# Kernel optimization log

Measured on AMD Instinct MI355X. Metric: run time of the kernel, lower is better.

Reference implementation:

```python
import jax, jax.numpy as jnp
import numpy as np

N_NODES = 50000
N_EDGES = 800000
D_IN = 128
D_HID = 200
D_OUT = 64
EPS = 0.0  # initial_eps, train_eps=False


def setup_inputs() -> dict:
    key = jax.random.key(0)
    ks = jax.random.split(key, 8)
    x = jax.random.normal(ks[0], (N_NODES, D_IN), dtype=jnp.float32)
    edge_row = jax.random.randint(ks[1], (N_EDGES,), 0, N_NODES)
    edge_col = jax.random.randint(ks[2], (N_EDGES,), 0, N_NODES)
    edge_val = jax.random.uniform(ks[3], (N_EDGES,), dtype=jnp.float32)
    W1 = jax.random.normal(ks[4], (D_IN, D_HID), dtype=jnp.float32) * 0.05
    b1 = jnp.zeros((D_HID,), dtype=jnp.float32)
    W2 = jax.random.normal(ks[5], (D_HID, D_OUT), dtype=jnp.float32) * 0.05
    b2 = jnp.zeros((D_OUT,), dtype=jnp.float32)
    return {"x": x, "edge_row": edge_row, "edge_col": edge_col,
            "edge_val": edge_val, "W1": W1, "b1": b1, "W2": W2, "b2": b2}


def reference(x, edge_row, edge_col, edge_val, W1, b1, W2, b2):
    # SpMM: agg[i] = sum_e val[e] * x[col[e]] for edges with row[e] == i
    msgs = edge_val[:, None] * x[edge_col]            # [E, D_IN] gather
    agg = jax.ops.segment_sum(msgs, edge_row, num_segments=N_NODES)  # [N, D_IN]
    # (1 + eps) * x + A @ x, then 2-layer MLP (Linear -> ReLU -> Linear)
    h = (1.0 + EPS) * x + agg
    h = jax.nn.relu(h @ W1 + b1)                      # [N, D_HID]
    out = h @ W2 + b2                                 # [N, D_OUT]
    return out
```

## Files before the change

### kernel.cpp

```cpp
#include <hip/hip_runtime.h>

#define NN 50000
#define NE 800000
#define DIN 128
#define DH 200
#define DHP 256
#define DO 64
#define RPB 32
#define NBUCK 1564
#define CAP 1024
#define EPB 4096
#define NBLK_E ((NE + EPB - 1) / EPB)
#define CVT_B 3125
#define PACK_B 24
#define NBIN 256

typedef float f32x4 __attribute__((ext_vector_type(4)));
typedef short bf16x8 __attribute__((ext_vector_type(8)));
typedef short s16x4 __attribute__((ext_vector_type(4)));
typedef unsigned int uint;

__device__ __forceinline__ unsigned short f2bf(float f) {
  unsigned int b = __float_as_uint(f);
  b = (b + 0x7FFFu + ((b >> 16) & 1u)) >> 16;
  return (unsigned short)b;
}
__device__ __forceinline__ float bf2f(unsigned short u) {
  return __uint_as_float((unsigned int)u << 16);
}

__global__ __launch_bounds__(256) void k_prep(const float* __restrict__ x,
                                              uint* __restrict__ xb,
                                              const int* __restrict__ row,
                                              int* __restrict__ hist,
                                              const float* __restrict__ W1,
                                              const float* __restrict__ W2,
                                              unsigned short* __restrict__ B1p,
                                              unsigned short* __restrict__ B2p) {
  __shared__ int lh[NBUCK];
  const int bid = blockIdx.x;
  const int tid = threadIdx.x;
  if (bid < CVT_B) {
    int i = bid * 256 + tid;
    f32x4 a = *reinterpret_cast<const f32x4*>(x + (size_t)i * 8);
    f32x4 b = *reinterpret_cast<const f32x4*>(x + (size_t)i * 8 + 4);
    uint4 o;
    o.x = (uint)f2bf(a[0]) | ((uint)f2bf(a[1]) << 16);
    o.y = (uint)f2bf(a[2]) | ((uint)f2bf(a[3]) << 16);
    o.z = (uint)f2bf(b[0]) | ((uint)f2bf(b[1]) << 16);
    o.w = (uint)f2bf(b[2]) | ((uint)f2bf(b[3]) << 16);
    *reinterpret_cast<uint4*>(xb + (size_t)i * 4) = o;
  } else if (bid < CVT_B + NBLK_E) {
    const int hb = bid - CVT_B;
    const int e0 = hb * EPB;
    for (int j = tid; j < NBUCK; j += 256) lh[j] = 0;
    __syncthreads();
#pragma unroll
    for (int p = 0; p < EPB / 256; ++p) {
      int e = e0 + p * 256 + tid;
      if (e < NE) atomicAdd(&lh[row[e] / RPB], 1);
    }
    __syncthreads();
    int* hrow = hist + (size_t)hb * NBUCK;
    for (int j = tid; j < NBUCK; j += 256) hrow[j] = lh[j];
  } else {
    int gidx = (bid - CVT_B - NBLK_E) * 256 + tid;
    if (gidx < 4096) {
      int idx = gidx;
      int lane = idx & 63;
      int s = (idx >> 6) & 3;
      int t = idx >> 8;
      int n = t * 16 + (lane & 15);
      unsigned short v[8];
#pragma unroll
      for (int j = 0; j < 8; ++j) {
        int k = s * 32 + (j & 3) + ((lane >> 4) << 2) + ((j >> 2) << 4);
        float f = (n < DH) ? W1[(size_t)k * DH + n] : 0.f;
        v[j] = f2bf(f);
      }
      *reinterpret_cast<uint4*>(B1p + (size_t)idx * 8) =
          *reinterpret_cast<const uint4*>(v);
    } else {
      int idx = gidx - 4096;
      int lane = idx & 63;
      int s = (idx >> 6) & 7;
      int t = idx >> 9;
      int n = t * 16 + (lane & 15);
      unsigned short v[8];
#pragma unroll
      for (int j = 0; j < 8; ++j) {
        int k = s * 32 + (j & 3) + ((lane >> 4) << 2) + ((j >> 2) << 4);
        float f = (k < DH) ? W2[(size_t)k * DO + n] : 0.f;
        v[j] = f2bf(f);
      }
      *reinterpret_cast<uint4*>(B2p + (size_t)idx * 8) =
          *reinterpret_cast<const uint4*>(v);
    }
  }
}

__global__ __launch_bounds__(256) void k_scanB(int* __restrict__ hist,
                                               int* __restrict__ cnt) {
  __shared__ int ws[4];
  const int k = blockIdx.x;
  const int tid = threadIdx.x;
  int v = (tid < NBLK_E) ? hist[(size_t)tid * NBUCK + k] : 0;
  int lane = tid & 63, wid = tid >> 6;
  int incl = v;
#pragma unroll
  for (int d = 1; d < 64; d <<= 1) {
    int t = __shfl_up(incl, d, 64);
    if (lane >= d) incl += t;
  }
  if (lane == 63) ws[wid] = incl;
  __syncthreads();
  if (tid == 0) {
    int s = 0;
#pragma unroll
    for (int q = 0; q < 4; ++q) { int xx = ws[q]; ws[q] = s; s += xx; }
  }
  __syncthreads();
  int excl = ws[wid] + incl - v;
  if (tid < NBLK_E) hist[(size_t)tid * NBUCK + k] = excl;
  if (tid == 255) cnt[k] = excl;
}

__global__ __launch_bounds__(256) void k_scatC(const int* __restrict__ row,
                                               const int* __restrict__ col,
                                               const float* __restrict__ val,
                                               const int* __restrict__ hist,
                                               uint2* __restrict__ ep) {
  __shared__ int lh[NBUCK];
  __shared__ int lbase[NBUCK];
  const int tid = threadIdx.x;
  const int e0 = blockIdx.x * EPB;
  const int* hrow = hist + (size_t)blockIdx.x * NBUCK;
  for (int j = tid; j < NBUCK; j += 256) { lh[j] = 0; lbase[j] = hrow[j]; }
  __syncthreads();
#pragma unroll
  for (int p = 0; p < EPB / 256; ++p) {
    int e = e0 + p * 256 + tid;
    if (e < NE) {
      int r = row[e];
      int k = r / RPB;
      int rank = atomicAdd(&lh[k], 1);
      int pos = lbase[k] + rank;
      if (pos < CAP)
        ep[(size_t)k * CAP + pos] =
            make_uint2((uint)col[e] | ((uint)(r & (RPB - 1)) << 16),
                       __float_as_uint(val[e]));
    }
  }
}

__global__ __launch_bounds__(256, 8) void k_spmm_mlp(const uint* __restrict__ xbu,
                                                     const uint2* __restrict__ ep,
                                                     const int* __restrict__ cnt,
                                                     const unsigned short* __restrict__ B1p,
                                                     const float* __restrict__ b1,
                                                     const unsigned short* __restrict__ B2p,
                                                     const float* __restrict__ b2,
                                                     float* __restrict__ out) {
  __shared__ uint2 buf2[2112];
  __shared__ int deg2[NBIN], rbase2[NBIN], rpos2[NBIN];
  __shared__ int ws[4];
  uint2* se = buf2;
  unsigned short* hb = (unsigned short*)(buf2 + CAP);
  unsigned short* hs = (unsigned short*)buf2;
  const int tid = threadIdx.x;
  const int bucket = blockIdx.x;
  const int r0 = bucket * RPB;
  const int w = tid >> 6, lane = tid & 63;
  const int g = lane >> 4, r16 = lane & 15;
  const int half = lane >> 5, l32 = lane & 31;

  deg2[tid] = 0;
  __syncthreads();

  int n = cnt[bucket];
  if (n > CAP) n = CAP;
  const uint2* eb = ep + (size_t)bucket * CAP;

  uint2 rec[4];
  int key[4];
#pragma unroll
  for (int q = 0; q < 4; ++q) {
    int j = q * 256 + tid;
    rec[q] = (j < n) ? eb[j] : make_uint2(0u, 0u);
    key[q] = (int)(((rec[q].x >> 16) & (RPB - 1)) * 8 + ((rec[q].x & 0xFFFFu) >> 13));
  }
#pragma unroll
  for (int q = 0; q < 4; ++q)
    if (q * 256 + tid < n) atomicAdd(&deg2[key[q]], 1);
  __syncthreads();

  {
    int v = deg2[tid];
    int incl = v;
#pragma unroll
    for (int d = 1; d < 64; d <<= 1) {
      int t = __shfl_up(incl, d, 64);
      if (lane >= d) incl += t;
    }
    if (lane == 63) ws[w] = incl;
    __syncthreads();
    if (tid == 0) {
      int s = 0;
#pragma unroll
      for (int q = 0; q < 4; ++q) { int xx = ws[q]; ws[q] = s; s += xx; }
    }
    __syncthreads();
    int excl = ws[w] + incl - v;
    rbase2[tid] = excl;
    rpos2[tid] = excl;
  }
  __syncthreads();

#pragma unroll
  for (int q = 0; q < 4; ++q)
    if (q * 256 + tid < n) {
      int p = atomicAdd(&rpos2[key[q]], 1);
      se[p] = make_uint2(rec[q].x & 0xFFFFu, rec[q].y);
    }
  __syncthreads();

  const uint2* xb2 = reinterpret_cast<const uint2*>(xbu);
  for (int rr = w; rr < RPB; rr += 4) {
    int gr = r0 + rr;
    if (gr >= NN) {
      if (half == 0)
        *reinterpret_cast<uint2*>(&hb[rr * 136 + 4 * l32]) = make_uint2(0u, 0u);
      continue;
    }
    int s = rbase2[rr * 8];
    int en = (rr < RPB - 1) ? rbase2[(rr + 1) * 8] : n;
    float a0 = 0.f, a1 = 0.f, a2 = 0.f, a3 = 0.f;
    int j = s + half;
    for (; j + 6 < en; j += 8) {
      uint2 e0 = se[j], e1 = se[j + 2], e2 = se[j + 4], e3 = se[j + 6];
      uint2 q0 = xb2[(size_t)e0.x * 32 + l32];
      uint2 q1 = xb2[(size_t)e1.x * 32 + l32];
      uint2 q2 = xb2[(size_t)e2.x * 32 + l32];
      uint2 q3 = xb2[(size_t)e3.x * 32 + l32];
      float v0 = __uint_as_float(e0.y), v1 = __uint_as_float(e1.y);
      float v2 = __uint_as_float(e2.y), v3 = __uint_as_float(e3.y);
      a0 += v0 * bf2f((unsigned short)q0.x) + v1 * bf2f((unsigned short)q1.x) +
            v2 * bf2f((unsigned short)q2.x) + v3 * bf2f((unsigned short)q3.x);
      a1 += v0 * bf2f((unsigned short)(q0.x >> 16)) + v1 * bf2f((unsigned short)(q1.x >> 16)) +
            v2 * bf2f((unsigned short)(q2.x >> 16)) + v3 * bf2f((unsigned short)(q3.x >> 16));
      a2 += v0 * bf2f((unsigned short)q0.y) + v1 * bf2f((unsigned short)q1.y) +
            v2 * bf2f((unsigned short)q2.y) + v3 * bf2f((unsigned short)q3.y);
      a3 += v0 * bf2f((unsigned short)(q0.y >> 16)) + v1 * bf2f((unsigned short)(q1.y >> 16)) +
            v2 * bf2f((unsigned short)(q2.y >> 16)) + v3 * bf2f((unsigned short)(q3.y >> 16));
    }
    for (; j < en; j += 2) {
      uint2 e0 = se[j];
      uint2 q0 = xb2[(size_t)e0.x * 32 + l32];
      float v0 = __uint_as_float(e0.y);
      a0 += v0 * bf2f((unsigned short)q0.x);
      a1 += v0 * bf2f((unsigned short)(q0.x >> 16));
      a2 += v0 * bf2f((unsigned short)q0.y);
      a3 += v0 * bf2f((unsigned short)(q0.y >> 16));
    }
    a0 += __shfl_xor(a0, 32, 64);
    a1 += __shfl_xor(a1, 32, 64);
    a2 += __shfl_xor(a2, 32, 64);
    a3 += __shfl_xor(a3, 32, 64);
    uint2 xs = xb2[(size_t)gr * 32 + l32];
    a0 += bf2f((unsigned short)xs.x);
    a1 += bf2f((unsigned short)(xs.x >> 16));
    a2 += bf2f((unsigned short)xs.y);
    a3 += bf2f((unsigned short)(xs.y >> 16));
    if (half == 0) {
      uint2 o;
      o.x = (uint)f2bf(a0) | ((uint)f2bf(a1) << 16);
      o.y = (uint)f2bf(a2) | ((uint)f2bf(a3) << 16);
      *reinterpret_cast<uint2*>(&hb[rr * 136 + 4 * l32]) = o;
    }
  }
  __syncthreads();

  f32x4 acc[2][4];
#pragma unroll
  for (int a = 0; a < 2; ++a)
#pragma unroll
    for (int b = 0; b < 4; ++b)
#pragma unroll
      for (int c = 0; c < 4; ++c) acc[a][b][c] = 0.f;

  for (int s = 0; s < 4; ++s) {
    bf16x8 af[2];
#pragma unroll
    for (int mr = 0; mr < 2; ++mr) {
      const unsigned short* p = &hb[(mr * 16 + r16) * 136 + s * 32 + g * 4];
      s16x4 lo4 = *reinterpret_cast<const s16x4*>(p);
      s16x4 hi4 = *reinterpret_cast<const s16x4*>(p + 16);
#pragma unroll
      for (int j = 0; j < 4; ++j) { af[mr][j] = lo4[j]; af[mr][4 + j] = hi4[j]; }
    }
#pragma unroll
    for (int nr = 0; nr < 4; ++nr) {
      int t = w * 4 + nr;
      bf16x8 bf = *reinterpret_cast<const bf16x8*>(B1p + (size_t)((t * 4 + s) * 64 + lane) * 8);
      acc[0][nr] = __builtin_amdgcn_mfma_f32_16x16x32_bf16(af[0], bf, acc[0][nr], 0, 0, 0);
      acc[1][nr] = __builtin_amdgcn_mfma_f32_16x16x32_bf16(af[1], bf, acc[1][nr], 0, 0, 0);
    }
  }
  __syncthreads();
#pragma unroll
  for (int mr = 0; mr < 2; ++mr)
#pragma unroll
    for (int nr = 0; nr < 4; ++nr) {
      int nn = w * 64 + nr * 16 + r16;
      float bias = (nn < DH) ? b1[nn] : 0.f;
#pragma unroll
      for (int i = 0; i < 4; ++i) {
        int rl = mr * 16 + g * 4 + i;
        float v = acc[mr][nr][i] + bias;
        v = v > 0.f ? v : 0.f;
        if (nn >= DH) v = 0.f;
        hs[rl * 260 + nn] = f2bf(v);
      }
    }
  __syncthreads();

  f32x4 acc2[2];
#pragma unroll
  for (int b = 0; b < 2; ++b)
#pragma unroll
    for (int c = 0; c < 4; ++c) acc2[b][c] = 0.f;

  for (int s = 0; s < 8; ++s) {
#pragma unroll
    for (int mt = 0; mt < 2; ++mt) {
      const unsigned short* p = &hs[(mt * 16 + r16) * 260 + s * 32 + g * 4];
      s16x4 lo4 = *reinterpret_cast<const s16x4*>(p);
      s16x4 hi4 = *reinterpret_cast<const s16x4*>(p + 16);
      bf16x8 af;
#pragma unroll
      for (int j = 0; j < 4; ++j) { af[j] = lo4[j]; af[4 + j] = hi4[j]; }
      bf16x8 bf = *reinterpret_cast<const bf16x8*>(B2p + (size_t)((w * 8 + s) * 64 + lane) * 8);
      acc2[mt] = __builtin_amdgcn_mfma_f32_16x16x32_bf16(af, bf, acc2[mt], 0, 0, 0);
    }
  }
#pragma unroll
  for (int mt = 0; mt < 2; ++mt) {
    int nn = w * 16 + r16;
    float bias = b2[nn];
#pragma unroll
    for (int i = 0; i < 4; ++i) {
      int grow = r0 + mt * 16 + g * 4 + i;
      if (grow < NN) out[(size_t)grow * DO + nn] = acc2[mt][i] + bias;
    }
  }
}

extern "C" void kernel_launch(void* const* d_in, const int* in_sizes, int n_in,
                              void* d_out, int out_size, void* d_ws, size_t ws_size,
                              hipStream_t stream) {
  const float* x = (const float*)d_in[0];
  const int* erow = (const int*)d_in[1];
  const int* ecol = (const int*)d_in[2];
  const float* eval_ = (const float*)d_in[3];
  const float* W1 = (const float*)d_in[4];
  const float* b1 = (const float*)d_in[5];
  const float* W2 = (const float*)d_in[6];
  const float* b2 = (const float*)d_in[7];
  float* out = (float*)d_out;

  char* ws = (char*)d_ws;
  size_t o = 0;
  uint* xb = (uint*)(ws + o);          o += (size_t)NN * 64 * 4;
  unsigned short* B1p = (unsigned short*)(ws + o); o += 32768 * 2;
  unsigned short* B2p = (unsigned short*)(ws + o); o += 16384 * 2;
  o = (o + 255) & ~(size_t)255;
  int* cnt = (int*)(ws + o);           o += (NBUCK * 4 + 255) & ~(size_t)255;
  int* hist = (int*)(ws + o);          o += (size_t)NBLK_E * NBUCK * 4;
  o = (o + 255) & ~(size_t)255;
  uint2* ep = (uint2*)(ws + o);

  k_prep<<<CVT_B + NBLK_E + PACK_B, 256, 0, stream>>>(x, xb, erow, hist, W1, W2, B1p, B2p);
  k_scanB<<<NBUCK, 256, 0, stream>>>(hist, cnt);
  k_scatC<<<NBLK_E, 256, 0, stream>>>(erow, ecol, eval_, hist, ep);
  k_spmm_mlp<<<NBUCK, 256, 0, stream>>>(xb, ep, cnt, B1p, b1, B2p, b2, out);
}
```

Before: 79.15 us.

## Fuse histogram, scan and scatter into one kernel using global atomic bucket offsets

Result: slower. 85.29 us (+7.8%).

```diff
diff --git a/kernel.cpp b/kernel.cpp
--- a/kernel.cpp
+++ b/kernel.cpp
@@ -9,7 +9,7 @@
 #define RPB 32
 #define NBUCK 1564
 #define CAP 1024
-#define EPB 4096
+#define EPB 8192
 #define NBLK_E ((NE + EPB - 1) / EPB)
 #define CVT_B 3125
 #define PACK_B 24
@@ -19,6 +19,7 @@
 typedef short bf16x8 __attribute__((ext_vector_type(8)));
 typedef short s16x4 __attribute__((ext_vector_type(4)));
 typedef unsigned int uint;
+typedef unsigned long long u64;
 
 __device__ __forceinline__ unsigned short f2bf(float f) {
   unsigned int b = __float_as_uint(f);
@@ -29,19 +30,55 @@
   return __uint_as_float((unsigned int)u << 16);
 }
 
-__global__ __launch_bounds__(256) void k_prep(const float* __restrict__ x,
-                                              uint* __restrict__ xb,
-                                              const int* __restrict__ row,
-                                              int* __restrict__ hist,
-                                              const float* __restrict__ W1,
-                                              const float* __restrict__ W2,
-                                              unsigned short* __restrict__ B1p,
-                                              unsigned short* __restrict__ B2p) {
+__global__ __launch_bounds__(256) void k_build(const float* __restrict__ x,
+                                               uint* __restrict__ xb,
+                                               const int* __restrict__ row,
+                                               const int* __restrict__ col,
+                                               const float* __restrict__ val,
+                                               int* __restrict__ cnt,
+                                               uint2* __restrict__ ep,
+                                               const float* __restrict__ W1,
+                                               const float* __restrict__ W2,
+                                               unsigned short* __restrict__ B1p,
+                                               unsigned short* __restrict__ B2p) {
   __shared__ int lh[NBUCK];
+  __shared__ int lbase[NBUCK];
   const int bid = blockIdx.x;
   const int tid = threadIdx.x;
-  if (bid < CVT_B) {
-    int i = bid * 256 + tid;
+
+  if (bid < NBLK_E) {
+    const int e0 = bid * EPB;
+    for (int j = tid; j < NBUCK; j += 256) lh[j] = 0;
+    __syncthreads();
+#pragma unroll 4
+    for (int p = 0; p < EPB / 256; ++p) {
+      int e = e0 + p * 256 + tid;
+      if (e < NE) atomicAdd(&lh[row[e] >> 5], 1);
+    }
+    __syncthreads();
+    for (int k = tid; k < NBUCK; k += 256) {
+      int c = lh[k];
+      lbase[k] = c ? atomicAdd(&cnt[k], c) : 0;
+      lh[k] = 0;
+    }
+    __syncthreads();
+#pragma unroll 4
+    for (int p = 0; p < EPB / 256; ++p) {
+      int e = e0 + p * 256 + tid;
+      if (e < NE) {
+        int r = row[e];
+        int k = r >> 5;
+        int rank = atomicAdd(&lh[k], 1);
+        int pos = lbase[k] + rank;
+        if (pos < CAP) {
+          u64 rv = ((u64)__float_as_uint(val[e]) << 32) |
+                   (uint)((uint)col[e] | ((uint)(r & (RPB - 1)) << 16));
+          __builtin_nontemporal_store(rv, (u64*)&ep[(size_t)k * CAP + pos]);
+        }
+      }
+    }
+  } else if (bid < NBLK_E + CVT_B) {
+    int i = (bid - NBLK_E) * 256 + tid;
     f32x4 a = *reinterpret_cast<const f32x4*>(x + (size_t)i * 8);
     f32x4 b = *reinterpret_cast<const f32x4*>(x + (size_t)i * 8 + 4);
     uint4 o;
@@ -50,21 +87,8 @@
     o.z = (uint)f2bf(b[0]) | ((uint)f2bf(b[1]) << 16);
     o.w = (uint)f2bf(b[2]) | ((uint)f2bf(b[3]) << 16);
     *reinterpret_cast<uint4*>(xb + (size_t)i * 4) = o;
-  } else if (bid < CVT_B + NBLK_E) {
-    const int hb = bid - CVT_B;
-    const int e0 = hb * EPB;
-    for (int j = tid; j < NBUCK; j += 256) lh[j] = 0;
-    __syncthreads();
-#pragma unroll
-    for (int p = 0; p < EPB / 256; ++p) {
-      int e = e0 + p * 256 + tid;
-      if (e < NE) atomicAdd(&lh[row[e] / RPB], 1);
-    }
-    __syncthreads();
-    int* hrow = hist + (size_t)hb * NBUCK;
-    for (int j = tid; j < NBUCK; j += 256) hrow[j] = lh[j];
   } else {
-    int gidx = (bid - CVT_B - NBLK_E) * 256 + tid;
+    int gidx = (bid - NBLK_E - CVT_B) * 256 + tid;
     if (gidx < 4096) {
       int idx = gidx;
       int lane = idx & 63;
@@ -80,7 +104,7 @@
       }
       *reinterpret_cast<uint4*>(B1p + (size_t)idx * 8) =
           *reinterpret_cast<const uint4*>(v);
-    } else {
+    } else if (gidx < 6144) {
       int idx = gidx - 4096;
       int lane = idx & 63;
       int s = (idx >> 6) & 7;
@@ -95,60 +119,6 @@
       }
       *reinterpret_cast<uint4*>(B2p + (size_t)idx * 8) =
           *reinterpret_cast<const uint4*>(v);
-    }
-  }
-}
-
-__global__ __launch_bounds__(256) void k_scanB(int* __restrict__ hist,
-                                               int* __restrict__ cnt) {
-  __shared__ int ws[4];
-  const int k = blockIdx.x;
-  const int tid = threadIdx.x;
-  int v = (tid < NBLK_E) ? hist[(size_t)tid * NBUCK + k] : 0;
-  int lane = tid & 63, wid = tid >> 6;
-  int incl = v;
-#pragma unroll
-  for (int d = 1; d < 64; d <<= 1) {
-    int t = __shfl_up(incl, d, 64);
-    if (lane >= d) incl += t;
-  }
-  if (lane == 63) ws[wid] = incl;
-  __syncthreads();
-  if (tid == 0) {
-    int s = 0;
-#pragma unroll
-    for (int q = 0; q < 4; ++q) { int xx = ws[q]; ws[q] = s; s += xx; }
-  }
-  __syncthreads();
-  int excl = ws[wid] + incl - v;
-  if (tid < NBLK_E) hist[(size_t)tid * NBUCK + k] = excl;
-  if (tid == 255) cnt[k] = excl;
-}
-
-__global__ __launch_bounds__(256) void k_scatC(const int* __restrict__ row,
-                                               const int* __restrict__ col,
-                                               const float* __restrict__ val,
-                                               const int* __restrict__ hist,
-                                               uint2* __restrict__ ep) {
-  __shared__ int lh[NBUCK];
-  __shared__ int lbase[NBUCK];
-  const int tid = threadIdx.x;
-  const int e0 = blockIdx.x * EPB;
-  const int* hrow = hist + (size_t)blockIdx.x * NBUCK;
-  for (int j = tid; j < NBUCK; j += 256) { lh[j] = 0; lbase[j] = hrow[j]; }
-  __syncthreads();
-#pragma unroll
-  for (int p = 0; p < EPB / 256; ++p) {
-    int e = e0 + p * 256 + tid;
-    if (e < NE) {
-      int r = row[e];
-      int k = r / RPB;
-      int rank = atomicAdd(&lh[k], 1);
-      int pos = lbase[k] + rank;
-      if (pos < CAP)
-        ep[(size_t)k * CAP + pos] =
-            make_uint2((uint)col[e] | ((uint)(r & (RPB - 1)) << 16),
-                       __float_as_uint(val[e]));
     }
   }
 }
@@ -237,21 +207,19 @@
     float a0 = 0.f, a1 = 0.f, a2 = 0.f, a3 = 0.f;
     int j = s + half;
     for (; j + 6 < en; j += 8) {
-      uint2 e0 = se[j], e1 = se[j + 2], e2 = se[j + 4], e3 = se[j + 6];
-      uint2 q0 = xb2[(size_t)e0.x * 32 + l32];
-      uint2 q1 = xb2[(size_t)e1.x * 32 + l32];
-      uint2 q2 = xb2[(size_t)e2.x * 32 + l32];
-      uint2 q3 = xb2[(size_t)e3.x * 32 + l32];
-      float v0 = __uint_as_float(e0.y), v1 = __uint_as_float(e1.y);
-      float v2 = __uint_as_float(e2.y), v3 = __uint_as_float(e3.y);
-      a0 += v0 * bf2f((unsigned short)q0.x) + v1 * bf2f((unsigned short)q1.x) +
-            v2 * bf2f((unsigned short)q2.x) + v3 * bf2f((unsigned short)q3.x);
-      a1 += v0 * bf2f((unsigned short)(q0.x >> 16)) + v1 * bf2f((unsigned short)(q1.x >> 16)) +
-            v2 * bf2f((unsigned short)(q2.x >> 16)) + v3 * bf2f((unsigned short)(q3.x >> 16));
-      a2 += v0 * bf2f((unsigned short)q0.y) + v1 * bf2f((unsigned short)q1.y) +
-            v2 * bf2f((unsigned short)q2.y) + v3 * bf2f((unsigned short)q3.y);
-      a3 += v0 * bf2f((unsigned short)(q0.y >> 16)) + v1 * bf2f((unsigned short)(q1.y >> 16)) +
-            v2 * bf2f((unsigned short)(q2.y >> 16)) + v3 * bf2f((unsigned short)(q3.y >> 16));
+      uint2 e[4], qv[4];
+#pragma unroll
+      for (int t = 0; t < 4; ++t) e[t] = se[j + 2 * t];
+#pragma unroll
+      for (int t = 0; t < 4; ++t) qv[t] = xb2[(size_t)e[t].x * 32 + l32];
+#pragma unroll
+      for (int t = 0; t < 4; ++t) {
+        float v = __uint_as_float(e[t].y);
+        a0 += v * bf2f((unsigned short)qv[t].x);
+        a1 += v * bf2f((unsigned short)(qv[t].x >> 16));
+        a2 += v * bf2f((unsigned short)qv[t].y);
+        a3 += v * bf2f((unsigned short)(qv[t].y >> 16));
+      }
     }
     for (; j < en; j += 2) {
       uint2 e0 = se[j];
@@ -375,12 +343,10 @@
   unsigned short* B2p = (unsigned short*)(ws + o); o += 16384 * 2;
   o = (o + 255) & ~(size_t)255;
   int* cnt = (int*)(ws + o);           o += (NBUCK * 4 + 255) & ~(size_t)255;
-  int* hist = (int*)(ws + o);          o += (size_t)NBLK_E * NBUCK * 4;
-  o = (o + 255) & ~(size_t)255;
   uint2* ep = (uint2*)(ws + o);
 
-  k_prep<<<CVT_B + NBLK_E + PACK_B, 256, 0, stream>>>(x, xb, erow, hist, W1, W2, B1p, B2p);
-  k_scanB<<<NBUCK, 256, 0, stream>>>(hist, cnt);
-  k_scatC<<<NBLK_E, 256, 0, stream>>>(erow, ecol, eval_, hist, ep);
+  hipMemsetAsync(cnt, 0, (size_t)NBUCK * sizeof(int), stream);
+  k_build<<<NBLK_E + CVT_B + PACK_B, 256, 0, stream>>>(
+      x, xb, erow, ecol, eval_, cnt, ep, W1, W2, B1p, B2p);
   k_spmm_mlp<<<NBUCK, 256, 0, stream>>>(xb, ep, cnt, B1p, b1, B2p, b2, out);
 }
```
